# Performance work log

Measured on AMD Instinct MI355X. Metric: run time of the kernel, lower is better.

The kernel has to match this reference:

```python
import jax, jax.numpy as jnp
import numpy as np

N = 50000
E = 800000
HID = 128
HEADS = 3
OPH = (HID + HEADS - 1) // HEADS  # 43
MID = OPH * HEADS                 # 129
OUT = 6


def _gat_layer(x, src, dst, W, a_src, a_dst, b, heads, ch, concat, num_nodes):
    # x: [N, F_in]; W: [F_in, heads*ch]; a_src/a_dst: [heads, ch]; b: [heads*ch] or [ch]
    h = (x @ W).reshape(num_nodes, heads, ch)          # [N, H, C]
    al = jnp.einsum('nhc,hc->nh', h, a_src)            # [N, H]
    ar = jnp.einsum('nhc,hc->nh', h, a_dst)            # [N, H]
    e = jax.nn.leaky_relu(al[src] + ar[dst], 0.2)      # [E, H]
    emax = jax.ops.segment_max(e, dst, num_segments=num_nodes)
    emax = jnp.where(jnp.isfinite(emax), emax, 0.0)
    ex = jnp.exp(e - emax[dst])                        # [E, H]
    denom = jax.ops.segment_sum(ex, dst, num_segments=num_nodes)
    alpha = ex / (denom[dst] + 1e-16)                  # [E, H]
    msg = h[src] * alpha[:, :, None]                   # [E, H, C]
    out = jax.ops.segment_sum(msg, dst, num_segments=num_nodes)  # [N, H, C]
    out = out.reshape(num_nodes, heads * ch) if concat else out.mean(axis=1)
    return out + b


def setup_inputs() -> dict:
    key = jax.random.key(0)
    ks = jax.random.split(key, 16)
    x = jax.random.normal(ks[0], (N, HID), dtype=jnp.float32)
    edge_index = jax.random.randint(ks[1], (2, E), 0, N, dtype=jnp.int64)
    s = 0.1
    return {
        'x': x, 'edge_index': edge_index,
        'W0': jax.random.normal(ks[2], (HID, HEADS * OPH), jnp.float32) * s,
        'a0s': jax.random.normal(ks[3], (HEADS, OPH), jnp.float32) * s,
        'a0d': jax.random.normal(ks[4], (HEADS, OPH), jnp.float32) * s,
        'b0': jnp.zeros((HEADS * OPH,), jnp.float32),
        'W1': jax.random.normal(ks[5], (MID, HEADS * OPH), jnp.float32) * s,
        'a1s': jax.random.normal(ks[6], (HEADS, OPH), jnp.float32) * s,
        'a1d': jax.random.normal(ks[7], (HEADS, OPH), jnp.float32) * s,
        'b1': jnp.zeros((HEADS * OPH,), jnp.float32),
        'W2': jax.random.normal(ks[8], (MID, OUT), jnp.float32) * s,
        'a2s': jax.random.normal(ks[9], (1, OUT), jnp.float32) * s,
        'a2d': jax.random.normal(ks[10], (1, OUT), jnp.float32) * s,
        'b2': jnp.zeros((OUT,), jnp.float32),
    }


def reference(x, edge_index, W0, a0s, a0d, b0, W1, a1s, a1d, b1, W2, a2s, a2d, b2):
    # add self loops (GATConv add_self_loops=True)
    loops = jnp.arange(N, dtype=edge_index.dtype)
    src = jnp.concatenate([edge_index[0], loops])
    dst = jnp.concatenate([edge_index[1], loops])
    h = _gat_layer(x, src, dst, W0, a0s, a0d, b0, HEADS, OPH, True, N)
    h = jax.nn.leaky_relu(h, 0.2)
    h = _gat_layer(h, src, dst, W1, a1s, a1d, b1, HEADS, OPH, True, N)
    h = jax.nn.leaky_relu(h, 0.2)
    out = _gat_layer(h, src, dst, W2, a2s, a2d, b2, 1, OUT, False, N)
    return out
```

## Files before the change

### kernel.cpp

```cpp
#include <hip/hip_runtime.h>

#define N_NODES 50000
#define N_EDGES 800000
#define ET (N_EDGES + N_NODES)
#define MID 129
#define OUTC 6
#define NB 196
#define CT 4096

typedef _Float16 half2v __attribute__((ext_vector_type(2)));
typedef _Float16 half8  __attribute__((ext_vector_type(8)));
typedef float    floatx4 __attribute__((ext_vector_type(4)));

__device__ __forceinline__ float lrelu(float x) { return fmaxf(x, 0.2f * x); }


__global__ void ccount_kernel(const int* __restrict__ dst, int* __restrict__ ccnt) {
    __shared__ int lh[NB];
    for (int i = threadIdx.x; i < NB; i += 256) lh[i] = 0;
    __syncthreads();
    int base = blockIdx.x * CT;
#pragma unroll 4
    for (int j = 0; j < CT; j += 256) {
        int e = base + j + threadIdx.x;
        if (e < ET) {
            int d = (e < N_EDGES) ? dst[e] : (e - N_EDGES);
            atomicAdd(&lh[d >> 8], 1);
        }
    }
    __syncthreads();
    for (int i = threadIdx.x; i < NB; i += 256) {
        int v = lh[i];
        if (v) atomicAdd(&ccnt[i], v);
    }
}

__global__ void cscan_kernel(const int* __restrict__ ccnt, int* __restrict__ cbase,
                             int* __restrict__ ccur) {
    __shared__ int buf[256];
    int t = threadIdx.x;
    buf[t] = (t < NB) ? ccnt[t] : 0;
    __syncthreads();
    for (int off = 1; off < 256; off <<= 1) {
        int v = (t >= off) ? buf[t - off] : 0;
        __syncthreads();
        buf[t] += v;
        __syncthreads();
    }
    int excl = t ? buf[t - 1] : 0;
    if (t < NB) { cbase[t] = excl; ccur[t] = excl; }
    if (t == NB - 1) cbase[NB] = buf[t];
}

__global__ void cscatter_kernel(const int* __restrict__ src, const int* __restrict__ dst,
                                int* __restrict__ ccur, unsigned int* __restrict__ cval) {
    __shared__ unsigned int staged[CT];
    __shared__ int lh[NB], lex[NB], lcur[NB], lgb[NB];
    __shared__ int sbuf[256];
    int tid = threadIdx.x;
    for (int i = tid; i < NB; i += 256) lh[i] = 0;
    __syncthreads();
    int base = blockIdx.x * CT;
    unsigned int myv[16];
    int myb[16];
    int myn = 0;
#pragma unroll
    for (int j = 0; j < 16; ++j) {
        int e = base + j * 256 + tid;
        if (e < ET) {
            int s, d;
            if (e < N_EDGES) { s = src[e]; d = dst[e]; }
            else             { s = d = e - N_EDGES; }
            int b = d >> 8;
            myv[j] = ((unsigned)b << 24) | ((unsigned)(d & 255) << 16) | (unsigned)s;
            myb[j] = b;
            atomicAdd(&lh[b], 1);
            myn = j + 1;
        }
    }
    __syncthreads();
    sbuf[tid] = (tid < NB) ? lh[tid] : 0;
    __syncthreads();
    for (int off = 1; off < 256; off <<= 1) {
        int v = (tid >= off) ? sbuf[tid - off] : 0;
        __syncthreads();
        sbuf[tid] += v;
        __syncthreads();
    }
    if (tid < NB) {
        int excl = tid ? sbuf[tid - 1] : 0;
        lex[tid] = excl;
        lcur[tid] = excl;
    }
    __syncthreads();
    for (int j = 0; j < myn; ++j) {
        int p = atomicAdd(&lcur[myb[j]], 1);
        staged[p] = myv[j];
    }
    __syncthreads();
    if (tid < NB) {
        int c = lh[tid];
        lgb[tid] = c ? atomicAdd(&ccur[tid], c) : 0;
    }
    __syncthreads();
    int tot = ET - base; if (tot > CT) tot = CT;
    for (int i = tid; i < tot; i += 256) {
        unsigned int v = staged[i];
        int b = v >> 24;
        cval[lgb[b] + (i - lex[b])] = v;
    }
}

__global__ __launch_bounds__(512)
void fine_kernel(const unsigned int* __restrict__ cval, const int* __restrict__ cbase,
                 int* __restrict__ rowp, unsigned short* __restrict__ csr_src) {
    __shared__ int h[256], cur[256], sb[256];
    int b = blockIdx.x;
    int beg = cbase[b], end = cbase[b + 1];
    int t = threadIdx.x;
    if (t < 256) h[t] = 0;
    __syncthreads();
    for (int i = beg + t; i < end; i += 512)
        atomicAdd(&h[(cval[i] >> 16) & 255], 1);
    __syncthreads();
    if (t < 256) sb[t] = h[t];
    __syncthreads();
    for (int off = 1; off < 256; off <<= 1) {
        int v = 0;
        if (t < 256 && t >= off) v = sb[t - off];
        __syncthreads();
        if (t < 256) sb[t] += v;
        __syncthreads();
    }
    if (t < 256) {
        int excl = t ? sb[t - 1] : 0;
        cur[t] = excl;
        int dstv = (b << 8) + t;
        if (dstv <= N_NODES) rowp[dstv] = beg + excl;
    }
    __syncthreads();
    for (int i = beg + t; i < end; i += 512) {
        unsigned int v = cval[i];
        int low = (v >> 16) & 255;
        int p = atomicAdd(&cur[low], 1);
        csr_src[beg + p] = (unsigned short)(v & 0xFFFFu);
    }
}

__global__ void padw_kernel(const float* __restrict__ W0, const float* __restrict__ a0s,
                            const float* __restrict__ a0d, const float* __restrict__ W1,
                            const float* __restrict__ a1s, const float* __restrict__ a1d,
                            _Float16* __restrict__ Wt0, _Float16* __restrict__ Wt1,
                            float* __restrict__ w128row1) {
    const int SEG = 144 * 128;
    int i = blockIdx.x * blockDim.x + threadIdx.x;
    if (i < 2 * SEG) {
        int l = i / SEG;
        int ii = i - l * SEG;
        int n = ii >> 7, k = ii & 127;
        const float* W = l ? W1 : W0;
        const float* as = l ? a1s : a0s;
        const float* ad = l ? a1d : a0d;
        float v = 0.f;
        if (n < 129) v = W[k * MID + n];
        else if (n < 132) {
            int h = n - 129;
            float sum = 0.f;
            for (int c = 0; c < 43; ++c) sum += W[k * MID + 43 * h + c] * as[43 * h + c];
            v = sum;
        } else if (n < 135) {
            int h = n - 132;
            float sum = 0.f;
            for (int c = 0; c < 43; ++c) sum += W[k * MID + 43 * h + c] * ad[43 * h + c];
            v = sum;
        }
        (l ? Wt1 : Wt0)[ii] = (_Float16)v;
    } else if (i < 2 * SEG + 144) {
        int n = i - 2 * SEG;
        float v = 0.f;
        if (n < 129) v = W1[128 * MID + n];
        else if (n < 132) {
            int h = n - 129;
            float sum = 0.f;
            for (int c = 0; c < 43; ++c) sum += W1[128 * MID + 43 * h + c] * a1s[43 * h + c];
            v = sum;
        } else if (n < 135) {
            int h = n - 132;
            float sum = 0.f;
            for (int c = 0; c < 43; ++c) sum += W1[128 * MID + 43 * h + c] * a1d[43 * h + c];
            v = sum;
        }
        w128row1[n] = v;
    }
}

template <bool SRC32, bool RANK1>
__global__ __launch_bounds__(256)
void gemm_mfma_kernel(const float* __restrict__ X32, const _Float16* __restrict__ Xh,
                      const float* __restrict__ Xl,
                      const _Float16* __restrict__ Wt, const float* __restrict__ w128,
                      _Float16* __restrict__ Hm16, float* __restrict__ Hl,
                      float* __restrict__ al, float* __restrict__ ar) {
    int wave = threadIdx.x >> 6, lane = threadIdx.x & 63;
    int mt = blockIdx.x * 4 + wave;
    if (mt * 16 >= N_NODES) return;
    int t = lane & 15, quad = lane >> 4;
    int row0 = mt * 16;

    half8 af[4];
    if (SRC32) {
        const float* arow = X32 + ((size_t)(row0 + t) << 7) + quad * 8;
#pragma unroll
        for (int kt = 0; kt < 4; ++kt) {
            float4 a0 = *(const float4*)(arow + kt * 32);
            float4 a1 = *(const float4*)(arow + kt * 32 + 4);
            half8 h;
            h[0] = (_Float16)a0.x; h[1] = (_Float16)a0.y;
            h[2] = (_Float16)a0.z; h[3] = (_Float16)a0.w;
            h[4] = (_Float16)a1.x; h[5] = (_Float16)a1.y;
            h[6] = (_Float16)a1.z; h[7] = (_Float16)a1.w;
            af[kt] = h;
        }
    } else {
        const _Float16* arow = Xh + ((size_t)(row0 + t) << 7) + quad * 8;
#pragma unroll
        for (int kt = 0; kt < 4; ++kt) af[kt] = *(const half8*)(arow + kt * 32);
    }

    floatx4 acc[3];
#pragma unroll
    for (int nt = 0; nt < 3; ++nt) {
        int ntile = blockIdx.y * 3 + nt;
        const _Float16* brow = Wt + ((size_t)(ntile * 16 + t) << 7) + quad * 8;
        floatx4 a = {0.f, 0.f, 0.f, 0.f};
#pragma unroll
        for (int kt = 0; kt < 4; ++kt) {
            half8 b = *(const half8*)(brow + kt * 32);
            a = __builtin_amdgcn_mfma_f32_16x16x32_f16(af[kt], b, a, 0, 0, 0);
        }
        acc[nt] = a;
    }

#pragma unroll
    for (int r = 0; r < 4; ++r) {
        int row = row0 + quad * 4 + r;
        float xl = RANK1 ? Xl[row] : 0.f;
#pragma unroll
        for (int nt = 0; nt < 3; ++nt) {
            int n = (blockIdx.y * 3 + nt) * 16 + t;
            float v = acc[nt][r];
            if (RANK1) v += xl * w128[n];
            if (n < 128) {
                Hm16[((size_t)row << 7) + n] = (_Float16)v;
            } else if (n == 128) {
                Hl[row] = v;
            } else if (n < 132) {
                al[row * 3 + (n - 129)] = v;
            } else if (n < 135) {
                ar[row * 3 + (n - 132)] = v;
            }
        }
    }
}

template <bool ACT, bool L2EPI>
__global__ void agg129_kernel(const _Float16* __restrict__ Hm16, const float* __restrict__ Hl,
                              const float* __restrict__ al, const float* __restrict__ ar,
                              const int* __restrict__ rowp, const unsigned short* __restrict__ srcs,
                              const float* __restrict__ bias, _Float16* __restrict__ Omh,
                              float* __restrict__ Ol,
                              const float* __restrict__ W2, const float* __restrict__ a2s,
                              const float* __restrict__ a2d, float* __restrict__ H2,
                              float* __restrict__ al2, float* __restrict__ ar2) {
    __shared__ float4 exs[4][64];
    int lane = threadIdx.x & 63;
    int wv   = threadIdx.x >> 6;
    int wid  = blockIdx.x * 4 + wv;
    if (wid >= N_NODES) return;

    int beg = rowp[wid], end = rowp[wid + 1];
    float ard0 = ar[wid * 3], ard1 = ar[wid * 3 + 1], ard2 = ar[wid * 3 + 2];

    int g  = lane >> 4;
    int q  = lane & 15;
    int cb = 8 * q;

    bool bm0[8], bm1[8];
#pragma unroll
    for (int j = 0; j < 8; ++j) {
        bm0[j] = (cb + j) < 43;
        bm1[j] = (cb + j) < 86;
    }
    unsigned selv[4];
#pragma unroll
    for (int p = 0; p < 4; ++p) {
        int c0 = cb + 2 * p, c1 = c0 + 1;
        int l0 = (c0 < 43) ? 4 : (c0 < 86) ? 6 : 0;
        int l1 = (c1 < 43) ? 4 : (c1 < 86) ? 6 : 0;
        selv[p] = (unsigned)l0 | ((unsigned)(l0 + 1) << 8) |
                  ((unsigned)l1 << 16) | ((unsigned)(l1 + 1) << 24);
    }

    float accv[8];
#pragma unroll
    for (int j = 0; j < 8; ++j) accv[j] = 0.f;
    float acc128 = 0.f;
    float s0 = 0.f, s1 = 0.f, s2 = 0.f;
    float4* exw = exs[wv];

    for (int base = beg; base < end; base += 64) {
        int i = base + lane;
        float e0 = 0.f, e1 = 0.f, e2 = 0.f;
        int s = 0;
        if (i < end) {
            s = (int)srcs[i];
            const float* ap = al + s * 3;
            e0 = __expf(lrelu(ap[0] + ard0));
            e1 = __expf(lrelu(ap[1] + ard1));
            e2 = __expf(lrelu(ap[2] + ard2));
            s0 += e0; s1 += e1; s2 += e2;
        }
        exw[lane] = make_float4(e0, e1, e2, __int_as_float(s));
        int cnt = end - base; if (cnt > 64) cnt = 64;
        for (int tt = 0; tt < cnt; tt += 4) {
            float4 ed = exw[tt + g];
            int ss = __float_as_int(ed.w);
            half8 hv = *(const half8*)(Hm16 + ((size_t)ss << 7) + cb);
            unsigned p01 = __builtin_bit_cast(unsigned, __builtin_amdgcn_cvt_pkrtz(ed.x, ed.y));
            unsigned p2z = __builtin_bit_cast(unsigned, __builtin_amdgcn_cvt_pkrtz(ed.z, ed.z));
            if (q == 0) acc128 += ed.z * Hl[ss];
#pragma unroll
            for (int p = 0; p < 4; ++p) {
                unsigned wp = __builtin_amdgcn_perm(p01, p2z, selv[p]);
                half2v w2 = __builtin_bit_cast(half2v, wp);
                accv[2 * p]     += (float)w2[0] * (float)hv[2 * p];
                accv[2 * p + 1] += (float)w2[1] * (float)hv[2 * p + 1];
            }
        }
    }
#pragma unroll
    for (int off = 16; off <= 32; off <<= 1) {
#pragma unroll
        for (int j = 0; j < 8; ++j) accv[j] += __shfl_xor(accv[j], off, 64);
        acc128 += __shfl_xor(acc128, off, 64);
    }
#pragma unroll
    for (int off = 32; off; off >>= 1) {
        s0 += __shfl_xor(s0, off, 64);
        s1 += __shfl_xor(s1, off, 64);
        s2 += __shfl_xor(s2, off, 64);
    }
    float d0 = 1.f / (s0 + 1e-16f);
    float d1 = 1.f / (s1 + 1e-16f);
    float d2 = 1.f / (s2 + 1e-16f);
    if (g == 0) {
        float4 bv0 = *(const float4*)(bias + cb);
        float4 bv1 = *(const float4*)(bias + cb + 4);
        float bb[8] = {bv0.x, bv0.y, bv0.z, bv0.w, bv1.x, bv1.y, bv1.z, bv1.w};
        float o[8];
#pragma unroll
        for (int j = 0; j < 8; ++j) {
            float dv = bm0[j] ? d0 : (bm1[j] ? d1 : d2);
            o[j] = accv[j] * dv + bb[j];
            if (ACT) o[j] = lrelu(o[j]);
        }
        float o128 = 0.f;
        if (lane == 0) {
            o128 = acc128 * d2 + bias[128];
            if (ACT) o128 = lrelu(o128);
        }
        if (!L2EPI) {
            half8 oh;
#pragma unroll
            for (int j = 0; j < 8; ++j) oh[j] = (_Float16)o[j];
            *(half8*)(Omh + ((size_t)wid << 7) + cb) = oh;
            if (lane == 0) Ol[wid] = o128;
        } else {
            float pr[OUTC];
#pragma unroll
            for (int c = 0; c < OUTC; ++c) pr[c] = 0.f;
#pragma unroll
            for (int j = 0; j < 8; ++j) {
                const float* wr = W2 + (cb + j) * OUTC;
                float ov = o[j];
#pragma unroll
                for (int c = 0; c < OUTC; ++c) pr[c] += ov * wr[c];
            }
            if (lane == 0) {
#pragma unroll
                for (int c = 0; c < OUTC; ++c) pr[c] += o128 * W2[128 * OUTC + c];
            }
#pragma unroll
            for (int off = 1; off < 16; off <<= 1)
#pragma unroll
                for (int c = 0; c < OUTC; ++c) pr[c] += __shfl_xor(pr[c], off, 64);
            if (lane == 0) {
                float sl = 0.f, sr = 0.f;
#pragma unroll
                for (int c = 0; c < OUTC; ++c) {
                    H2[wid * OUTC + c] = pr[c];
                    sl += pr[c] * a2s[c];
                    sr += pr[c] * a2d[c];
                }
                al2[wid] = sl;
                ar2[wid] = sr;
            }
        }
    }
}

__global__ void agg6_kernel(const float* __restrict__ H2, const float* __restrict__ al2,
                            const float* __restrict__ ar2, const int* __restrict__ rowp,
                            const unsigned short* __restrict__ srcs, const float* __restrict__ b2,
                            float* __restrict__ out) {
    __shared__ float2 exs[4][64];
    int lane = threadIdx.x & 63;
    int wv   = threadIdx.x >> 6;
    int wid  = blockIdx.x * 4 + wv;
    if (wid >= N_NODES) return;
    int beg = rowp[wid], end = rowp[wid + 1];
    float ard = ar2[wid];
    int grp = lane >> 3;
    int myc = lane & 7;
    int cc  = (myc < OUTC) ? myc : 0;
    float ssum = 0.f, acc = 0.f;
    float2* exw = exs[wv];
    for (int base = beg; base < end; base += 64) {
        int i = base + lane;
        float ex = 0.f;
        int s = 0;
        if (i < end) {
            s = (int)srcs[i];
            ex = __expf(lrelu(al2[s] + ard));
            ssum += ex;
        }
        exw[lane] = make_float2(ex, __int_as_float(s));
        int cnt = end - base; if (cnt > 64) cnt = 64;
        for (int t = 0; t < cnt; t += 8) {
            float2 ed = exw[t + grp];
            int ss = __float_as_int(ed.y);
            acc += ed.x * H2[ss * OUTC + cc];
        }
    }
    acc += __shfl_xor(acc, 8, 64);
    acc += __shfl_xor(acc, 16, 64);
    acc += __shfl_xor(acc, 32, 64);
#pragma unroll
    for (int off = 32; off; off >>= 1) ssum += __shfl_xor(ssum, off, 64);
    float dinv = 1.f / (ssum + 1e-16f);
    if (lane < OUTC) out[(size_t)wid * OUTC + lane] = acc * dinv + b2[lane];
}


extern "C" void kernel_launch(void* const* d_in, const int* in_sizes, int n_in,
                              void* d_out, int out_size, void* d_ws, size_t ws_size,
                              hipStream_t stream) {
    const float* x   = (const float*)d_in[0];
    const int*   ei  = (const int*)d_in[1];
    const float* W0  = (const float*)d_in[2];
    const float* a0s = (const float*)d_in[3];
    const float* a0d = (const float*)d_in[4];
    const float* b0  = (const float*)d_in[5];
    const float* W1  = (const float*)d_in[6];
    const float* a1s = (const float*)d_in[7];
    const float* a1d = (const float*)d_in[8];
    const float* b1  = (const float*)d_in[9];
    const float* W2  = (const float*)d_in[10];
    const float* a2s = (const float*)d_in[11];
    const float* a2d = (const float*)d_in[12];
    const float* b2  = (const float*)d_in[13];
    float* out = (float*)d_out;

    char* p = (char*)d_ws;
    auto take = [&](size_t bytes) -> void* {
        void* r = (void*)p;
        p += (bytes + 255) & ~(size_t)255;
        return r;
    };
    int*            ccnt     = (int*)take((size_t)NB * 4);
    int*            cbase    = (int*)take((size_t)(NB + 1) * 4);
    int*            ccur     = (int*)take((size_t)NB * 4);
    unsigned int*   cval     = (unsigned int*)take((size_t)ET * 4);
    int*            rowp     = (int*)take((size_t)(N_NODES + 1) * 4);
    unsigned short* csr_src  = (unsigned short*)take((size_t)ET * 2);
    float*          al       = (float*)take((size_t)N_NODES * 3 * 4);
    float*          ar       = (float*)take((size_t)N_NODES * 3 * 4);
    _Float16*       Hm16     = (_Float16*)take((size_t)N_NODES * 128 * 2);
    _Float16*       Omh      = (_Float16*)take((size_t)N_NODES * 128 * 2);
    float*          Hl       = (float*)take((size_t)N_NODES * 4);
    float*          Ol       = (float*)take((size_t)N_NODES * 4);
    _Float16*       Wt0      = (_Float16*)take((size_t)144 * 128 * 2);
    _Float16*       Wt1      = (_Float16*)take((size_t)144 * 128 * 2);
    float*          w128row1 = (float*)take((size_t)144 * 4);
    float*          H2       = (float*)take((size_t)N_NODES * OUTC * 4);
    float*          al2      = (float*)take((size_t)N_NODES * 4);
    float*          ar2      = (float*)take((size_t)N_NODES * 4);

    const int* esrc = ei;
    const int* edst = ei + N_EDGES;

    hipMemsetAsync(ccnt, 0, (size_t)NB * 4, stream);
    const int cgrid = (ET + CT - 1) / CT;
    ccount_kernel<<<cgrid, 256, 0, stream>>>(edst, ccnt);
    cscan_kernel<<<1, 256, 0, stream>>>(ccnt, cbase, ccur);
    cscatter_kernel<<<cgrid, 256, 0, stream>>>(esrc, edst, ccur, cval);
    fine_kernel<<<NB, 512, 0, stream>>>(cval, cbase, rowp, csr_src);

    padw_kernel<<<(2 * 144 * 128 + 144 + 255) / 256, 256, 0, stream>>>(
        W0, a0s, a0d, W1, a1s, a1d, Wt0, Wt1, w128row1);

    const dim3 gemm_grid((N_NODES / 16 + 3) / 4, 3);
    const int  node_grid = (N_NODES + 3) / 4;

    gemm_mfma_kernel<true, false><<<gemm_grid, 256, 0, stream>>>(
        x, (const _Float16*)nullptr, Ol, Wt0, w128row1, Hm16, Hl, al, ar);
    agg129_kernel<true, false><<<node_grid, 256, 0, stream>>>(
        Hm16, Hl, al, ar, rowp, csr_src, b0, Omh, Ol,
        nullptr, nullptr, nullptr, nullptr, nullptr, nullptr);

    gemm_mfma_kernel<false, true><<<gemm_grid, 256, 0, stream>>>(
        (const float*)nullptr, Omh, Ol, Wt1, w128row1, Hm16, Hl, al, ar);
    agg129_kernel<true, true><<<node_grid, 256, 0, stream>>>(
        Hm16, Hl, al, ar, rowp, csr_src, b1, (_Float16*)nullptr, (float*)nullptr,
        W2, a2s, a2d, H2, al2, ar2);

    agg6_kernel<<<node_grid, 256, 0, stream>>>(H2, al2, ar2, rowp, csr_src, b2, out);
}
```

Measured before the change: 300.1 us.

## Map multiple destination nodes per wavefront in aggregation kernels and pad attention logits

The aggregation kernels now give each 16-lane quarter-wave its own destination node in the 129-channel layer, and each 8-lane group its own node in the 6-channel layer, instead of one node per 64-lane wave. With average degree around 17, the old mapping left many lanes idle and spent time on cross-group reductions. The al/ar attention logits are padded to a stride of 4 so each node's values load as a single float4. In exchange, each node's edges are processed serially within its lane group, so high-degree nodes become longer chains and load imbalance grows. The padded logit arrays also use more memory.

```diff
diff --git a/kernel.cpp b/kernel.cpp
--- a/kernel.cpp
+++ b/kernel.cpp
@@ -200,7 +200,7 @@
                       const float* __restrict__ Xl,
                       const _Float16* __restrict__ Wt, const float* __restrict__ w128,
                       _Float16* __restrict__ Hm16, float* __restrict__ Hl,
-                      float* __restrict__ al, float* __restrict__ ar) {
+                      float* __restrict__ al4, float* __restrict__ ar4) {
     int wave = threadIdx.x >> 6, lane = threadIdx.x & 63;
     int mt = blockIdx.x * 4 + wave;
     if (mt * 16 >= N_NODES) return;
@@ -255,9 +255,9 @@
             } else if (n == 128) {
                 Hl[row] = v;
             } else if (n < 132) {
-                al[row * 3 + (n - 129)] = v;
+                al4[row * 4 + (n - 129)] = v;
             } else if (n < 135) {
-                ar[row * 3 + (n - 132)] = v;
+                ar4[row * 4 + (n - 132)] = v;
             }
         }
     }
@@ -265,26 +265,28 @@
 
 template <bool ACT, bool L2EPI>
 __global__ void agg129_kernel(const _Float16* __restrict__ Hm16, const float* __restrict__ Hl,
-                              const float* __restrict__ al, const float* __restrict__ ar,
+                              const float* __restrict__ al4, const float* __restrict__ ar4,
                               const int* __restrict__ rowp, const unsigned short* __restrict__ srcs,
                               const float* __restrict__ bias, _Float16* __restrict__ Omh,
                               float* __restrict__ Ol,
                               const float* __restrict__ W2, const float* __restrict__ a2s,
                               const float* __restrict__ a2d, float* __restrict__ H2,
                               float* __restrict__ al2, float* __restrict__ ar2) {
-    __shared__ float4 exs[4][64];
+    __shared__ float4 exs[4][4][17];
     int lane = threadIdx.x & 63;
     int wv   = threadIdx.x >> 6;
-    int wid  = blockIdx.x * 4 + wv;
-    if (wid >= N_NODES) return;
-
-    int beg = rowp[wid], end = rowp[wid + 1];
-    float ard0 = ar[wid * 3], ard1 = ar[wid * 3 + 1], ard2 = ar[wid * 3 + 2];
-
-    int g  = lane >> 4;
-    int q  = lane & 15;
+    int qd   = lane >> 4;
+    int q    = lane & 15;
+    int wid  = ((blockIdx.x * 4 + wv) << 2) + qd;
+    bool active = wid < N_NODES;
+    int widc = active ? wid : 0;
+
+    int beg = 0, end = 0;
+    if (active) { beg = rowp[wid]; end = rowp[wid + 1]; }
+    float4 arv = *(const float4*)(ar4 + (size_t)widc * 4);
+    float ard0 = arv.x, ard1 = arv.y, ard2 = arv.z;
+
     int cb = 8 * q;
-
     bool bm0[8], bm1[8];
 #pragma unroll
     for (int j = 0; j < 8; ++j) {
@@ -306,24 +308,24 @@
     for (int j = 0; j < 8; ++j) accv[j] = 0.f;
     float acc128 = 0.f;
     float s0 = 0.f, s1 = 0.f, s2 = 0.f;
-    float4* exw = exs[wv];
-
-    for (int base = beg; base < end; base += 64) {
-        int i = base + lane;
+    float4* exq = exs[wv][qd];
+
+    for (int base = beg; base < end; base += 16) {
+        int i = base + q;
         float e0 = 0.f, e1 = 0.f, e2 = 0.f;
         int s = 0;
         if (i < end) {
             s = (int)srcs[i];
-            const float* ap = al + s * 3;
-            e0 = __expf(lrelu(ap[0] + ard0));
-            e1 = __expf(lrelu(ap[1] + ard1));
-            e2 = __expf(lrelu(ap[2] + ard2));
+            float4 av = *(const float4*)(al4 + (size_t)s * 4);
+            e0 = __expf(lrelu(av.x + ard0));
+            e1 = __expf(lrelu(av.y + ard1));
+            e2 = __expf(lrelu(av.z + ard2));
             s0 += e0; s1 += e1; s2 += e2;
         }
-        exw[lane] = make_float4(e0, e1, e2, __int_as_float(s));
-        int cnt = end - base; if (cnt > 64) cnt = 64;
-        for (int tt = 0; tt < cnt; tt += 4) {
-            float4 ed = exw[tt + g];
+        exq[q] = make_float4(e0, e1, e2, __int_as_float(s));
+        int cnt = end - base; if (cnt > 16) cnt = 16;
+        for (int t = 0; t < cnt; ++t) {
+            float4 ed = exq[t];
             int ss = __float_as_int(ed.w);
             half8 hv = *(const half8*)(Hm16 + ((size_t)ss << 7) + cb);
             unsigned p01 = __builtin_bit_cast(unsigned, __builtin_amdgcn_cvt_pkrtz(ed.x, ed.y));
@@ -339,13 +341,7 @@
         }
     }
 #pragma unroll
-    for (int off = 16; off <= 32; off <<= 1) {
-#pragma unroll
-        for (int j = 0; j < 8; ++j) accv[j] += __shfl_xor(accv[j], off, 64);
-        acc128 += __shfl_xor(acc128, off, 64);
-    }
-#pragma unroll
-    for (int off = 32; off; off >>= 1) {
+    for (int off = 1; off < 16; off <<= 1) {
         s0 += __shfl_xor(s0, off, 64);
         s1 += __shfl_xor(s1, off, 64);
         s2 += __shfl_xor(s2, off, 64);
@@ -353,58 +349,59 @@
     float d0 = 1.f / (s0 + 1e-16f);
     float d1 = 1.f / (s1 + 1e-16f);
     float d2 = 1.f / (s2 + 1e-16f);
-    if (g == 0) {
-        float4 bv0 = *(const float4*)(bias + cb);
-        float4 bv1 = *(const float4*)(bias + cb + 4);
-        float bb[8] = {bv0.x, bv0.y, bv0.z, bv0.w, bv1.x, bv1.y, bv1.z, bv1.w};
-        float o[8];
-#pragma unroll
-        for (int j = 0; j < 8; ++j) {
-            float dv = bm0[j] ? d0 : (bm1[j] ? d1 : d2);
-            o[j] = accv[j] * dv + bb[j];
-            if (ACT) o[j] = lrelu(o[j]);
-        }
-        float o128 = 0.f;
-        if (lane == 0) {
-            o128 = acc128 * d2 + bias[128];
-            if (ACT) o128 = lrelu(o128);
-        }
-        if (!L2EPI) {
+
+    float4 bv0 = *(const float4*)(bias + cb);
+    float4 bv1 = *(const float4*)(bias + cb + 4);
+    float bb[8] = {bv0.x, bv0.y, bv0.z, bv0.w, bv1.x, bv1.y, bv1.z, bv1.w};
+    float o[8];
+#pragma unroll
+    for (int j = 0; j < 8; ++j) {
+        float dv = bm0[j] ? d0 : (bm1[j] ? d1 : d2);
+        o[j] = accv[j] * dv + bb[j];
+        if (ACT) o[j] = lrelu(o[j]);
+    }
+    float o128 = 0.f;
+    if (q == 0) {
+        o128 = acc128 * d2 + bias[128];
+        if (ACT) o128 = lrelu(o128);
+    }
+    if (!L2EPI) {
+        if (active) {
             half8 oh;
 #pragma unroll
             for (int j = 0; j < 8; ++j) oh[j] = (_Float16)o[j];
             *(half8*)(Omh + ((size_t)wid << 7) + cb) = oh;
-            if (lane == 0) Ol[wid] = o128;
-        } else {
-            float pr[OUTC];
-#pragma unroll
-            for (int c = 0; c < OUTC; ++c) pr[c] = 0.f;
-#pragma unroll
-            for (int j = 0; j < 8; ++j) {
-                const float* wr = W2 + (cb + j) * OUTC;
-                float ov = o[j];
-#pragma unroll
-                for (int c = 0; c < OUTC; ++c) pr[c] += ov * wr[c];
+            if (q == 0) Ol[wid] = o128;
+        }
+    } else {
+        float pr[OUTC];
+#pragma unroll
+        for (int c = 0; c < OUTC; ++c) pr[c] = 0.f;
+#pragma unroll
+        for (int j = 0; j < 8; ++j) {
+            const float* wr = W2 + (cb + j) * OUTC;
+            float ov = o[j];
+#pragma unroll
+            for (int c = 0; c < OUTC; ++c) pr[c] += ov * wr[c];
+        }
+        if (q == 0) {
+#pragma unroll
+            for (int c = 0; c < OUTC; ++c) pr[c] += o128 * W2[128 * OUTC + c];
+        }
+#pragma unroll
+        for (int off = 1; off < 16; off <<= 1)
+#pragma unroll
+            for (int c = 0; c < OUTC; ++c) pr[c] += __shfl_xor(pr[c], off, 64);
+        if (active && q == 0) {
+            float sl = 0.f, sr = 0.f;
+#pragma unroll
+            for (int c = 0; c < OUTC; ++c) {
+                H2[wid * OUTC + c] = pr[c];
+                sl += pr[c] * a2s[c];
+                sr += pr[c] * a2d[c];
             }
-            if (lane == 0) {
-#pragma unroll
-                for (int c = 0; c < OUTC; ++c) pr[c] += o128 * W2[128 * OUTC + c];
-            }
-#pragma unroll
-            for (int off = 1; off < 16; off <<= 1)
-#pragma unroll
-                for (int c = 0; c < OUTC; ++c) pr[c] += __shfl_xor(pr[c], off, 64);
-            if (lane == 0) {
-                float sl = 0.f, sr = 0.f;
-#pragma unroll
-                for (int c = 0; c < OUTC; ++c) {
-                    H2[wid * OUTC + c] = pr[c];
-                    sl += pr[c] * a2s[c];
-                    sr += pr[c] * a2d[c];
-                }
-                al2[wid] = sl;
-                ar2[wid] = sr;
-            }
+            al2[wid] = sl;
+            ar2[wid] = sr;
         }
     }
 }
@@ -413,20 +410,22 @@
                             const float* __restrict__ ar2, const int* __restrict__ rowp,
                             const unsigned short* __restrict__ srcs, const float* __restrict__ b2,
                             float* __restrict__ out) {
-    __shared__ float2 exs[4][64];
+    __shared__ float2 exs[4][8][9];
     int lane = threadIdx.x & 63;
     int wv   = threadIdx.x >> 6;
-    int wid  = blockIdx.x * 4 + wv;
-    if (wid >= N_NODES) return;
-    int beg = rowp[wid], end = rowp[wid + 1];
-    float ard = ar2[wid];
-    int grp = lane >> 3;
-    int myc = lane & 7;
-    int cc  = (myc < OUTC) ? myc : 0;
+    int g8   = lane >> 3;
+    int c    = lane & 7;
+    int wid  = ((blockIdx.x * 4 + wv) << 3) + g8;
+    bool active = wid < N_NODES;
+    int widc = active ? wid : 0;
+    int beg = 0, end = 0;
+    if (active) { beg = rowp[wid]; end = rowp[wid + 1]; }
+    float ard = ar2[widc];
+    int cc = (c < OUTC) ? c : 0;
     float ssum = 0.f, acc = 0.f;
-    float2* exw = exs[wv];
-    for (int base = beg; base < end; base += 64) {
-        int i = base + lane;
+    float2* exq = exs[wv][g8];
+    for (int base = beg; base < end; base += 8) {
+        int i = base + c;
         float ex = 0.f;
         int s = 0;
         if (i < end) {
@@ -434,21 +433,18 @@
             ex = __expf(lrelu(al2[s] + ard));
             ssum += ex;
         }
-        exw[lane] = make_float2(ex, __int_as_float(s));
-        int cnt = end - base; if (cnt > 64) cnt = 64;
-        for (int t = 0; t < cnt; t += 8) {
-            float2 ed = exw[t + grp];
+        exq[c] = make_float2(ex, __int_as_float(s));
+        int cnt = end - base; if (cnt > 8) cnt = 8;
+        for (int t = 0; t < cnt; ++t) {
+            float2 ed = exq[t];
             int ss = __float_as_int(ed.y);
             acc += ed.x * H2[ss * OUTC + cc];
         }
     }
-    acc += __shfl_xor(acc, 8, 64);
-    acc += __shfl_xor(acc, 16, 64);
-    acc += __shfl_xor(acc, 32, 64);
-#pragma unroll
-    for (int off = 32; off; off >>= 1) ssum += __shfl_xor(ssum, off, 64);
+#pragma unroll
+    for (int off = 1; off < 8; off <<= 1) ssum += __shfl_xor(ssum, off, 64);
     float dinv = 1.f / (ssum + 1e-16f);
-    if (lane < OUTC) out[(size_t)wid * OUTC + lane] = acc * dinv + b2[lane];
+    if (active && c < OUTC) out[(size_t)wid * OUTC + c] = acc * dinv + b2[c];
 }
 
 
@@ -483,8 +479,8 @@
     unsigned int*   cval     = (unsigned int*)take((size_t)ET * 4);
     int*            rowp     = (int*)take((size_t)(N_NODES + 1) * 4);
     unsigned short* csr_src  = (unsigned short*)take((size_t)ET * 2);
-    float*          al       = (float*)take((size_t)N_NODES * 3 * 4);
-    float*          ar       = (float*)take((size_t)N_NODES * 3 * 4);
+    float*          al4      = (float*)take((size_t)N_NODES * 4 * 4);
+    float*          ar4      = (float*)take((size_t)N_NODES * 4 * 4);
     _Float16*       Hm16     = (_Float16*)take((size_t)N_NODES * 128 * 2);
     _Float16*       Omh      = (_Float16*)take((size_t)N_NODES * 128 * 2);
     float*          Hl       = (float*)take((size_t)N_NODES * 4);
@@ -510,19 +506,20 @@
         W0, a0s, a0d, W1, a1s, a1d, Wt0, Wt1, w128row1);
 
     const dim3 gemm_grid((N_NODES / 16 + 3) / 4, 3);
-    const int  node_grid = (N_NODES + 3) / 4;
+    const int  agg129_grid = (N_NODES + 15) / 16;
+    const int  agg6_grid   = (N_NODES + 31) / 32;
 
     gemm_mfma_kernel<true, false><<<gemm_grid, 256, 0, stream>>>(
-        x, (const _Float16*)nullptr, Ol, Wt0, w128row1, Hm16, Hl, al, ar);
-    agg129_kernel<true, false><<<node_grid, 256, 0, stream>>>(
-        Hm16, Hl, al, ar, rowp, csr_src, b0, Omh, Ol,
+        x, (const _Float16*)nullptr, Ol, Wt0, w128row1, Hm16, Hl, al4, ar4);
+    agg129_kernel<true, false><<<agg129_grid, 256, 0, stream>>>(
+        Hm16, Hl, al4, ar4, rowp, csr_src, b0, Omh, Ol,
         nullptr, nullptr, nullptr, nullptr, nullptr, nullptr);
 
     gemm_mfma_kernel<false, true><<<gemm_grid, 256, 0, stream>>>(
-        (const float*)nullptr, Omh, Ol, Wt1, w128row1, Hm16, Hl, al, ar);
-    agg129_kernel<true, true><<<node_grid, 256, 0, stream>>>(
-        Hm16, Hl, al, ar, rowp, csr_src, b1, (_Float16*)nullptr, (float*)nullptr,
+        (const float*)nullptr, Omh, Ol, Wt1, w128row1, Hm16, Hl, al4, ar4);
+    agg129_kernel<true, true><<<agg129_grid, 256, 0, stream>>>(
+        Hm16, Hl, al4, ar4, rowp, csr_src, b1, (_Float16*)nullptr, (float*)nullptr,
         W2, a2s, a2d, H2, al2, ar2);
 
-    agg6_kernel<<<node_grid, 256, 0, stream>>>(H2, al2, ar2, rowp, csr_src, b2, out);
-}
+    agg6_kernel<<<agg6_grid, 256, 0, stream>>>(H2, al2, ar2, rowp, csr_src, b2, out);
+}
```

After: 280.5 us. 6.6% less time.
